# Performance work log

Measured on AMD Instinct MI355X. Metric: run time of the kernel, lower is better.

Reference implementation:

```python
import jax, jax.numpy as jnp
import numpy as np

B, L, S, D = 64, 1024, 8, 128  # batch, seq len, num_snapshots, feat dim


def setup_inputs() -> dict:
    key = jax.random.key(0)
    ks = jax.random.split(key, 12)
    src_ids = jax.random.randint(ks[0], (B, L), 0, 2000, dtype=jnp.int32)
    dst_ids = jax.random.randint(ks[1], (B, L), 0, 2000, dtype=jnp.int32)
    # snapshot ids are 1..S in the original code (indexing uses snaps - 1)
    src_snaps = jax.random.randint(ks[2], (B, L), 1, S + 1, dtype=jnp.int32)
    dst_snaps = jax.random.randint(ks[3], (B, L), 1, S + 1, dtype=jnp.int32)
    def lin(k, fan_in, shape):
        return jax.random.uniform(k, shape, jnp.float32, -1.0, 1.0) / np.sqrt(fan_in)
    params = {
        # AggregateSnapshots MLP: Linear(S, D) -> ReLU -> Linear(D, 2)
        'agg_w1': lin(ks[4], S, (S, D)), 'agg_b1': lin(ks[5], S, (D,)),
        'agg_w2': lin(ks[6], D, (D, 2)), 'agg_b2': lin(ks[7], D, (2,)),
        # neighbor_intersect_encode_layer: Linear(1, D) -> ReLU -> Linear(D, D)
        'enc_w1': lin(ks[8], 1, (1, D)), 'enc_b1': lin(ks[9], 1, (D,)),
        'enc_w2': lin(ks[10], D, (D, D)), 'enc_b2': lin(ks[11], D, (D,)),
    }
    return dict(src_padded_nodes_neighbor_ids=src_ids,
                dst_padded_nodes_neighbor_ids=dst_ids,
                src_padded_nodes_snapshots=src_snaps,
                dst_padded_nodes_snapshots=dst_snaps,
                num_snapshots=S, **params)


def _match_counts(ids_a, sn_a, ids_b, sn_b):
    # counts[i, j] = #{k : ids_b[i,k] == ids_a[i,j] and sn_b[i,k] == sn_a[i,j]}
    eq = (ids_a[:, :, None] == ids_b[:, None, :]) & (sn_a[:, :, None] == sn_b[:, None, :])
    return eq.sum(axis=-1).astype(jnp.float32)  # [B, L]


def _intersects(ids, sn, other_ids, other_sn, num_snapshots):
    self_cnt = _match_counts(ids, sn, ids, sn)            # [B, L]
    cross_cnt = _match_counts(ids, sn, other_ids, other_sn)
    valid = (ids != 0).astype(jnp.float32)                # padding rows stay zero
    oh = jax.nn.one_hot(sn - 1, num_snapshots, dtype=jnp.float32)  # [B, L, S]
    cnts = jnp.stack([self_cnt, cross_cnt], axis=2)       # [B, L, 2]
    return (cnts * valid[:, :, None])[..., None] * oh[:, :, None, :]  # [B, L, 2, S]


def _agg_mlp(x, w1, b1, w2, b2):
    # x: [B, L, 2, S] -> Linear(S,D) -> ReLU -> Linear(D,2) -> reshape(B,L,2,2) -> mean over dim 2
    h = jax.nn.relu(jnp.einsum('blcs,sd->blcd', x, w1) + b1)
    y = jnp.einsum('blcd,de->blce', h, w2) + b2           # [B, L, 2, 2]
    return y.mean(axis=2)                                 # [B, L, 2]


def _encode(y, w1, b1, w2, b2):
    # y: [B, L, 2] -> unsqueeze(-1) -> Linear(1,D) -> ReLU -> Linear(D,D) -> sum over dim 2
    h = jax.nn.relu(y[..., None] * w1[0] + b1)            # [B, L, 2, D]
    z = jnp.einsum('blcd,de->blce', h, w2) + b2
    return z.sum(axis=2)                                  # [B, L, D]


def reference(src_padded_nodes_neighbor_ids, dst_padded_nodes_neighbor_ids,
              src_padded_nodes_snapshots, dst_padded_nodes_snapshots, num_snapshots,
              agg_w1, agg_b1, agg_w2, agg_b2, enc_w1, enc_b1, enc_w2, enc_b2):
    src_int = _intersects(src_padded_nodes_neighbor_ids, src_padded_nodes_snapshots,
                          dst_padded_nodes_neighbor_ids, dst_padded_nodes_snapshots, num_snapshots)
    dst_self_cross = _intersects(dst_padded_nodes_neighbor_ids, dst_padded_nodes_snapshots,
                                 src_padded_nodes_neighbor_ids, src_padded_nodes_snapshots, num_snapshots)
    # dst layout: channel 0 = counts from src list, channel 1 = self counts
    dst_int = dst_self_cross[:, :, ::-1, :]
    src_snap_feat = _agg_mlp(src_int, agg_w1, agg_b1, agg_w2, agg_b2)
    dst_snap_feat = _agg_mlp(dst_int, agg_w1, agg_b1, agg_w2, agg_b2)
    src_feat = _encode(src_snap_feat, enc_w1, enc_b1, enc_w2, enc_b2)
    dst_feat = _encode(dst_snap_feat, enc_w1, enc_b1, enc_w2, enc_b2)
    return (src_feat, dst_feat)
```

## Files before the change

kernel.cpp:

```cpp
#include <hip/hip_runtime.h>


#define LSEQ 1024
#define NBATCH 64
#define DDIM 128
#define NKEYS 16384
#define CMAX 16

__global__ __launch_bounds__(1024) void count_kernel(
    const int* __restrict__ src_ids, const int* __restrict__ dst_ids,
    const int* __restrict__ src_sn,  const int* __restrict__ dst_sn,
    unsigned int* __restrict__ cnt_src, unsigned int* __restrict__ cnt_dst)
{
    __shared__ unsigned int hist[NKEYS];
    const int b = blockIdx.x;
    const int t = threadIdx.x;

    for (int i = t; i < NKEYS; i += 1024) hist[i] = 0u;
    __syncthreads();

    const int base = b * LSEQ;
    const int sid = src_ids[base + t];
    const int ssn = src_sn[base + t];
    const int did = dst_ids[base + t];
    const int dsn = dst_sn[base + t];

    unsigned int skey = (unsigned int)(sid * 8 + ((ssn - 1) & 7));
    unsigned int dkey = (unsigned int)(did * 8 + ((dsn - 1) & 7));
    if (skey >= NKEYS) skey = NKEYS - 1;
    if (dkey >= NKEYS) dkey = NKEYS - 1;

    atomicAdd(&hist[skey], 1u);
    atomicAdd(&hist[dkey], 65536u);
    __syncthreads();

    const unsigned int hs = hist[skey];
    const unsigned int hd = hist[dkey];
    const unsigned int s_self  = hs & 0xffffu, s_cross = hs >> 16;
    const unsigned int d_self  = hd >> 16,     d_cross = hd & 0xffffu;
    const unsigned int sv = (sid != 0) ? 1u : 0u;
    const unsigned int dv = (did != 0) ? 1u : 0u;

    cnt_src[base + t] = (s_self * sv) | ((s_cross * sv) << 11)
                        | ((unsigned int)((ssn - 1) & 7) << 22);
    cnt_dst[base + t] = (d_self * dv) | ((d_cross * dv) << 11)
                        | ((unsigned int)((dsn - 1) & 7) << 22);
}

__global__ __launch_bounds__(128) void table_kernel(
    const float* __restrict__ agg_w1, const float* __restrict__ agg_b1,
    const float* __restrict__ agg_w2, const float* __restrict__ agg_b2,
    const float* __restrict__ enc_w1, const float* __restrict__ enc_b1,
    const float* __restrict__ enc_w2, const float* __restrict__ enc_b2,
    float* __restrict__ table)
{
    const int bx = blockIdx.x;
    const int sn = bx >> 8;
    const int c0 = (bx >> 4) & 15;
    const int c1 = bx & 15;
    const int d  = threadIdx.x;

    __shared__ float red0[DDIM], red1[DDIM], g[DDIM];

    const float w1d = agg_w1[sn * DDIM + d];
    const float b1d = agg_b1[d];
    const float h = fmaxf((float)c0 * w1d + b1d, 0.0f)
                  + fmaxf((float)c1 * w1d + b1d, 0.0f);
    red0[d] = h * agg_w2[d * 2 + 0];
    red1[d] = h * agg_w2[d * 2 + 1];
    __syncthreads();
    for (int s = 64; s > 0; s >>= 1) {
        if (d < s) { red0[d] += red0[d + s]; red1[d] += red1[d + s]; }
        __syncthreads();
    }
    const float y0 = agg_b2[0] + 0.5f * red0[0];
    const float y1 = agg_b2[1] + 0.5f * red1[0];
    __syncthreads();

    const float w1e = enc_w1[d], b1e = enc_b1[d];
    g[d] = fmaxf(y0 * w1e + b1e, 0.0f) + fmaxf(y1 * w1e + b1e, 0.0f);
    __syncthreads();

    float acc = 2.0f * enc_b2[d];
    #pragma unroll 8
    for (int k = 0; k < DDIM; ++k)
        acc += g[k] * enc_w2[k * DDIM + d];
    table[bx * DDIM + d] = acc;
}

__global__ __launch_bounds__(256) void gather_kernel(
    const unsigned int* __restrict__ cnt_src,
    const unsigned int* __restrict__ cnt_dst,
    const float* __restrict__ table,
    const float* __restrict__ agg_w1, const float* __restrict__ agg_b1,
    const float* __restrict__ agg_w2, const float* __restrict__ agg_b2,
    const float* __restrict__ enc_w1, const float* __restrict__ enc_b1,
    const float* __restrict__ enc_w2, const float* __restrict__ enc_b2,
    float* __restrict__ out)
{
    const int gt   = blockIdx.x * 256 + threadIdx.x;
    const int unit = gt >> 5;
    const int q    = gt & 31;
    const int side = unit >> 16;
    const int idx  = unit & 65535;

    const unsigned int packed = side ? cnt_dst[idx] : cnt_src[idx];
    const unsigned int c0 = packed & 0x7FFu;
    const unsigned int c1 = (packed >> 11) & 0x7FFu;
    const unsigned int sn = (packed >> 22) & 7u;

    float4 v;
    if (c0 < CMAX && c1 < CMAX) {
        const float4* src = (const float4*)(table
            + ((sn * 256u + c0 * 16u + c1) * DDIM));
        v = src[q];
    } else {
        float s0 = 0.0f, s1 = 0.0f;
        for (int dd = 0; dd < DDIM; ++dd) {
            const float w1d = agg_w1[sn * DDIM + dd];
            const float b1d = agg_b1[dd];
            const float h = fmaxf((float)c0 * w1d + b1d, 0.0f)
                          + fmaxf((float)c1 * w1d + b1d, 0.0f);
            s0 += h * agg_w2[dd * 2 + 0];
            s1 += h * agg_w2[dd * 2 + 1];
        }
        const float y0 = agg_b2[0] + 0.5f * s0;
        const float y1 = agg_b2[1] + 0.5f * s1;
        float o0 = 2.0f * enc_b2[q * 4 + 0];
        float o1 = 2.0f * enc_b2[q * 4 + 1];
        float o2 = 2.0f * enc_b2[q * 4 + 2];
        float o3 = 2.0f * enc_b2[q * 4 + 3];
        for (int k = 0; k < DDIM; ++k) {
            const float w1e = enc_w1[k], b1e = enc_b1[k];
            const float gk = fmaxf(y0 * w1e + b1e, 0.0f)
                           + fmaxf(y1 * w1e + b1e, 0.0f);
            o0 += gk * enc_w2[k * DDIM + q * 4 + 0];
            o1 += gk * enc_w2[k * DDIM + q * 4 + 1];
            o2 += gk * enc_w2[k * DDIM + q * 4 + 2];
            o3 += gk * enc_w2[k * DDIM + q * 4 + 3];
        }
        v = make_float4(o0, o1, o2, o3);
    }
    ((float4*)out)[gt] = v;
}

extern "C" void kernel_launch(void* const* d_in, const int* in_sizes, int n_in,
                              void* d_out, int out_size, void* d_ws, size_t ws_size,
                              hipStream_t stream)
{
    const int* src_ids = (const int*)d_in[0];
    const int* dst_ids = (const int*)d_in[1];
    const int* src_sn  = (const int*)d_in[2];
    const int* dst_sn  = (const int*)d_in[3];
    const float* agg_w1 = (const float*)d_in[5];
    const float* agg_b1 = (const float*)d_in[6];
    const float* agg_w2 = (const float*)d_in[7];
    const float* agg_b2 = (const float*)d_in[8];
    const float* enc_w1 = (const float*)d_in[9];
    const float* enc_b1 = (const float*)d_in[10];
    const float* enc_w2 = (const float*)d_in[11];
    const float* enc_b2 = (const float*)d_in[12];
    float* out = (float*)d_out;

    unsigned int* cnt_src = (unsigned int*)d_ws;
    unsigned int* cnt_dst = cnt_src + NBATCH * LSEQ;
    float* table = (float*)(cnt_dst + NBATCH * LSEQ);

    count_kernel<<<NBATCH, 1024, 0, stream>>>(src_ids, dst_ids, src_sn, dst_sn,
                                              cnt_src, cnt_dst);
    table_kernel<<<8 * CMAX * CMAX, 128, 0, stream>>>(
        agg_w1, agg_b1, agg_w2, agg_b2, enc_w1, enc_b1, enc_w2, enc_b2, table);
    gather_kernel<<<(2 * NBATCH * LSEQ * 32) / 256, 256, 0, stream>>>(
        cnt_src, cnt_dst, table,
        agg_w1, agg_b1, agg_w2, agg_b2, enc_w1, enc_b1, enc_w2, enc_b2, out);
}
```

Baseline: 111.1 us.

## Fuse count, table and gather into one cooperative persistent kernel

Replaces the three launches with one cooperative kernel that runs three phases separated by grid syncs. The phases are: zero a global per-batch histogram and build the lookup table with one wave per entry, fill the histogram with global atomics, then gather. Counts are no longer packed into a staging buffer; the gather recomputes keys from the ids and reads the histogram directly. The goal is to remove launch overhead and serialization between kernels. In exchange it adds a 4 MB global histogram to zero, global-memory atomics in place of LDS atomics, and the cost of grid-wide barriers.

```diff
diff --git a/kernel.cpp b/kernel.cpp
--- a/kernel.cpp
+++ b/kernel.cpp
@@ -1,147 +1,219 @@
 #include <hip/hip_runtime.h>
-
-
-#define LSEQ 1024
-#define NBATCH 64
-#define DDIM 128
-#define NKEYS 16384
-#define CMAX 16
-
-__global__ __launch_bounds__(1024) void count_kernel(
-    const int* __restrict__ src_ids, const int* __restrict__ dst_ids,
-    const int* __restrict__ src_sn,  const int* __restrict__ dst_sn,
-    unsigned int* __restrict__ cnt_src, unsigned int* __restrict__ cnt_dst)
-{
-    __shared__ unsigned int hist[NKEYS];
-    const int b = blockIdx.x;
-    const int t = threadIdx.x;
-
-    for (int i = t; i < NKEYS; i += 1024) hist[i] = 0u;
-    __syncthreads();
-
-    const int base = b * LSEQ;
-    const int sid = src_ids[base + t];
-    const int ssn = src_sn[base + t];
-    const int did = dst_ids[base + t];
-    const int dsn = dst_sn[base + t];
-
-    unsigned int skey = (unsigned int)(sid * 8 + ((ssn - 1) & 7));
-    unsigned int dkey = (unsigned int)(did * 8 + ((dsn - 1) & 7));
-    if (skey >= NKEYS) skey = NKEYS - 1;
-    if (dkey >= NKEYS) dkey = NKEYS - 1;
-
-    atomicAdd(&hist[skey], 1u);
-    atomicAdd(&hist[dkey], 65536u);
-    __syncthreads();
-
-    const unsigned int hs = hist[skey];
-    const unsigned int hd = hist[dkey];
-    const unsigned int s_self  = hs & 0xffffu, s_cross = hs >> 16;
-    const unsigned int d_self  = hd >> 16,     d_cross = hd & 0xffffu;
-    const unsigned int sv = (sid != 0) ? 1u : 0u;
-    const unsigned int dv = (did != 0) ? 1u : 0u;
-
-    cnt_src[base + t] = (s_self * sv) | ((s_cross * sv) << 11)
-                        | ((unsigned int)((ssn - 1) & 7) << 22);
-    cnt_dst[base + t] = (d_self * dv) | ((d_cross * dv) << 11)
-                        | ((unsigned int)((dsn - 1) & 7) << 22);
-}
-
-__global__ __launch_bounds__(128) void table_kernel(
-    const float* __restrict__ agg_w1, const float* __restrict__ agg_b1,
-    const float* __restrict__ agg_w2, const float* __restrict__ agg_b2,
-    const float* __restrict__ enc_w1, const float* __restrict__ enc_b1,
-    const float* __restrict__ enc_w2, const float* __restrict__ enc_b2,
-    float* __restrict__ table)
-{
-    const int bx = blockIdx.x;
-    const int sn = bx >> 8;
-    const int c0 = (bx >> 4) & 15;
-    const int c1 = bx & 15;
-    const int d  = threadIdx.x;
-
-    __shared__ float red0[DDIM], red1[DDIM], g[DDIM];
-
-    const float w1d = agg_w1[sn * DDIM + d];
-    const float b1d = agg_b1[d];
-    const float h = fmaxf((float)c0 * w1d + b1d, 0.0f)
-                  + fmaxf((float)c1 * w1d + b1d, 0.0f);
-    red0[d] = h * agg_w2[d * 2 + 0];
-    red1[d] = h * agg_w2[d * 2 + 1];
-    __syncthreads();
-    for (int s = 64; s > 0; s >>= 1) {
-        if (d < s) { red0[d] += red0[d + s]; red1[d] += red1[d + s]; }
-        __syncthreads();
-    }
-    const float y0 = agg_b2[0] + 0.5f * red0[0];
-    const float y1 = agg_b2[1] + 0.5f * red1[0];
-    __syncthreads();
-
-    const float w1e = enc_w1[d], b1e = enc_b1[d];
-    g[d] = fmaxf(y0 * w1e + b1e, 0.0f) + fmaxf(y1 * w1e + b1e, 0.0f);
-    __syncthreads();
-
-    float acc = 2.0f * enc_b2[d];
-    #pragma unroll 8
-    for (int k = 0; k < DDIM; ++k)
-        acc += g[k] * enc_w2[k * DDIM + d];
-    table[bx * DDIM + d] = acc;
-}
-
-__global__ __launch_bounds__(256) void gather_kernel(
-    const unsigned int* __restrict__ cnt_src,
-    const unsigned int* __restrict__ cnt_dst,
-    const float* __restrict__ table,
-    const float* __restrict__ agg_w1, const float* __restrict__ agg_b1,
-    const float* __restrict__ agg_w2, const float* __restrict__ agg_b2,
-    const float* __restrict__ enc_w1, const float* __restrict__ enc_b1,
-    const float* __restrict__ enc_w2, const float* __restrict__ enc_b2,
-    float* __restrict__ out)
-{
-    const int gt   = blockIdx.x * 256 + threadIdx.x;
-    const int unit = gt >> 5;
-    const int q    = gt & 31;
-    const int side = unit >> 16;
-    const int idx  = unit & 65535;
-
-    const unsigned int packed = side ? cnt_dst[idx] : cnt_src[idx];
-    const unsigned int c0 = packed & 0x7FFu;
-    const unsigned int c1 = (packed >> 11) & 0x7FFu;
-    const unsigned int sn = (packed >> 22) & 7u;
-
-    float4 v;
-    if (c0 < CMAX && c1 < CMAX) {
-        const float4* src = (const float4*)(table
-            + ((sn * 256u + c0 * 16u + c1) * DDIM));
-        v = src[q];
-    } else {
-        float s0 = 0.0f, s1 = 0.0f;
-        for (int dd = 0; dd < DDIM; ++dd) {
-            const float w1d = agg_w1[sn * DDIM + dd];
-            const float b1d = agg_b1[dd];
+#include <hip/hip_cooperative_groups.h>
+
+namespace cg = cooperative_groups;
+
+
+#define LSEQ    1024
+#define NBATCH  64
+#define DDIM    128
+#define NKEYS   16384
+#define CMAX    16
+#define NTHREADS 256
+#define MAXBLOCKS 1024
+#define NUNITS  (2 * NBATCH * LSEQ)
+#define NQUADS  (NUNITS * (DDIM / 4))
+
+__device__ __forceinline__ void slow_path(
+    unsigned int c0, unsigned int c1, unsigned int snz, int q,
+    const float* __restrict__ agg_w1, const float* __restrict__ agg_b1,
+    const float* __restrict__ agg_w2, const float* __restrict__ agg_b2,
+    const float* __restrict__ enc_w1, const float* __restrict__ enc_b1,
+    const float* __restrict__ enc_w2, const float* __restrict__ enc_b2,
+    float4* v)
+{
+    float s0 = 0.0f, s1 = 0.0f;
+    for (int dd = 0; dd < DDIM; ++dd) {
+        const float w1d = agg_w1[snz * DDIM + dd];
+        const float b1d = agg_b1[dd];
+        const float h = fmaxf((float)c0 * w1d + b1d, 0.0f)
+                      + fmaxf((float)c1 * w1d + b1d, 0.0f);
+        s0 += h * agg_w2[dd * 2 + 0];
+        s1 += h * agg_w2[dd * 2 + 1];
+    }
+    const float y0 = agg_b2[0] + 0.5f * s0;
+    const float y1 = agg_b2[1] + 0.5f * s1;
+    float o0 = 2.0f * enc_b2[q * 4 + 0];
+    float o1 = 2.0f * enc_b2[q * 4 + 1];
+    float o2 = 2.0f * enc_b2[q * 4 + 2];
+    float o3 = 2.0f * enc_b2[q * 4 + 3];
+    for (int k = 0; k < DDIM; ++k) {
+        const float w1e = enc_w1[k], b1e = enc_b1[k];
+        const float gk = fmaxf(y0 * w1e + b1e, 0.0f)
+                       + fmaxf(y1 * w1e + b1e, 0.0f);
+        o0 += gk * enc_w2[k * DDIM + q * 4 + 0];
+        o1 += gk * enc_w2[k * DDIM + q * 4 + 1];
+        o2 += gk * enc_w2[k * DDIM + q * 4 + 2];
+        o3 += gk * enc_w2[k * DDIM + q * 4 + 3];
+    }
+    *v = make_float4(o0, o1, o2, o3);
+}
+
+__device__ __forceinline__ void phase_zero_table(
+    int tid, int stride,
+    const float* __restrict__ agg_w1, const float* __restrict__ agg_b1,
+    const float* __restrict__ agg_w2, const float* __restrict__ agg_b2,
+    const float* __restrict__ enc_w1, const float* __restrict__ enc_b1,
+    const float* __restrict__ enc_w2, const float* __restrict__ enc_b2,
+    unsigned int* __restrict__ hist, float* __restrict__ table)
+{
+    uint4* h4 = (uint4*)hist;
+    const uint4 z = make_uint4(0u, 0u, 0u, 0u);
+    for (int i = tid; i < (NBATCH * NKEYS) / 4; i += stride) h4[i] = z;
+
+    const int lane = threadIdx.x & 63;
+    const int nwaves = stride >> 6;
+    for (int r = tid >> 6; r < 8 * CMAX * CMAX; r += nwaves) {
+        const int sn = r >> 8;
+        const int c0 = (r >> 4) & 15;
+        const int c1 = r & 15;
+        float p0 = 0.0f, p1 = 0.0f;
+        #pragma unroll
+        for (int half = 0; half < 2; ++half) {
+            const int d = lane + half * 64;
+            const float w1d = agg_w1[sn * DDIM + d];
+            const float b1d = agg_b1[d];
             const float h = fmaxf((float)c0 * w1d + b1d, 0.0f)
                           + fmaxf((float)c1 * w1d + b1d, 0.0f);
-            s0 += h * agg_w2[dd * 2 + 0];
-            s1 += h * agg_w2[dd * 2 + 1];
-        }
-        const float y0 = agg_b2[0] + 0.5f * s0;
-        const float y1 = agg_b2[1] + 0.5f * s1;
-        float o0 = 2.0f * enc_b2[q * 4 + 0];
-        float o1 = 2.0f * enc_b2[q * 4 + 1];
-        float o2 = 2.0f * enc_b2[q * 4 + 2];
-        float o3 = 2.0f * enc_b2[q * 4 + 3];
+            p0 += h * agg_w2[d * 2 + 0];
+            p1 += h * agg_w2[d * 2 + 1];
+        }
+        #pragma unroll
+        for (int m = 32; m; m >>= 1) {
+            p0 += __shfl_xor(p0, m, 64);
+            p1 += __shfl_xor(p1, m, 64);
+        }
+        const float y0 = agg_b2[0] + 0.5f * p0;
+        const float y1 = agg_b2[1] + 0.5f * p1;
+        float a0 = 2.0f * enc_b2[lane];
+        float a1 = 2.0f * enc_b2[lane + 64];
+        #pragma unroll 4
         for (int k = 0; k < DDIM; ++k) {
             const float w1e = enc_w1[k], b1e = enc_b1[k];
             const float gk = fmaxf(y0 * w1e + b1e, 0.0f)
                            + fmaxf(y1 * w1e + b1e, 0.0f);
-            o0 += gk * enc_w2[k * DDIM + q * 4 + 0];
-            o1 += gk * enc_w2[k * DDIM + q * 4 + 1];
-            o2 += gk * enc_w2[k * DDIM + q * 4 + 2];
-            o3 += gk * enc_w2[k * DDIM + q * 4 + 3];
-        }
-        v = make_float4(o0, o1, o2, o3);
-    }
-    ((float4*)out)[gt] = v;
+            a0 += gk * enc_w2[k * DDIM + lane];
+            a1 += gk * enc_w2[k * DDIM + lane + 64];
+        }
+        table[r * DDIM + lane]      = a0;
+        table[r * DDIM + lane + 64] = a1;
+    }
+}
+
+__device__ __forceinline__ void phase_hist(
+    int tid, int stride,
+    const int* __restrict__ src_ids, const int* __restrict__ dst_ids,
+    const int* __restrict__ src_sn,  const int* __restrict__ dst_sn,
+    unsigned int* __restrict__ hist)
+{
+    for (int i = tid; i < NUNITS; i += stride) {
+        const int side = i >> 16;
+        const int idx  = i & 65535;
+        const int id = side ? dst_ids[idx] : src_ids[idx];
+        const int sn = side ? dst_sn[idx]  : src_sn[idx];
+        unsigned int key = (unsigned int)(id * 8 + ((sn - 1) & 7));
+        if (key >= NKEYS) key = NKEYS - 1;
+        atomicAdd(&hist[(idx >> 10) * NKEYS + key], side ? 65536u : 1u);
+    }
+}
+
+__device__ __forceinline__ void phase_gather(
+    int tid, int stride,
+    const int* __restrict__ src_ids, const int* __restrict__ dst_ids,
+    const int* __restrict__ src_sn,  const int* __restrict__ dst_sn,
+    const unsigned int* __restrict__ hist, const float* __restrict__ table,
+    const float* __restrict__ agg_w1, const float* __restrict__ agg_b1,
+    const float* __restrict__ agg_w2, const float* __restrict__ agg_b2,
+    const float* __restrict__ enc_w1, const float* __restrict__ enc_b1,
+    const float* __restrict__ enc_w2, const float* __restrict__ enc_b2,
+    float* __restrict__ out)
+{
+    float4* out4 = (float4*)out;
+    #pragma unroll 2
+    for (int gt = tid; gt < NQUADS; gt += stride) {
+        const int unit = gt >> 5;
+        const int q    = gt & 31;
+        const int side = unit >> 16;
+        const int idx  = unit & 65535;
+        const int id = side ? dst_ids[idx] : src_ids[idx];
+        const int sn = side ? dst_sn[idx]  : src_sn[idx];
+        const unsigned int snz = (unsigned int)((sn - 1) & 7);
+        unsigned int key = (unsigned int)(id * 8 + snz);
+        if (key >= NKEYS) key = NKEYS - 1;
+        const unsigned int h = hist[(idx >> 10) * NKEYS + key];
+        const unsigned int lo = h & 0xffffu, hi = h >> 16;
+        const unsigned int valid = (id != 0) ? 1u : 0u;
+        const unsigned int c0 = (side ? hi : lo) * valid;
+        const unsigned int c1 = (side ? lo : hi) * valid;
+
+        float4 v;
+        if (c0 < CMAX && c1 < CMAX) {
+            v = ((const float4*)(table
+                + ((snz * 16u + c0) * 16u + c1) * DDIM))[q];
+        } else {
+            slow_path(c0, c1, snz, q, agg_w1, agg_b1, agg_w2, agg_b2,
+                      enc_w1, enc_b1, enc_w2, enc_b2, &v);
+        }
+        out4[gt] = v;
+    }
+}
+
+__global__ __launch_bounds__(NTHREADS, 4) void fused_kernel(
+    const int* __restrict__ src_ids, const int* __restrict__ dst_ids,
+    const int* __restrict__ src_sn,  const int* __restrict__ dst_sn,
+    const float* __restrict__ agg_w1, const float* __restrict__ agg_b1,
+    const float* __restrict__ agg_w2, const float* __restrict__ agg_b2,
+    const float* __restrict__ enc_w1, const float* __restrict__ enc_b1,
+    const float* __restrict__ enc_w2, const float* __restrict__ enc_b2,
+    unsigned int* __restrict__ hist, float* __restrict__ table,
+    float* __restrict__ out)
+{
+    const int tid    = blockIdx.x * NTHREADS + threadIdx.x;
+    const int stride = gridDim.x * NTHREADS;
+
+    phase_zero_table(tid, stride, agg_w1, agg_b1, agg_w2, agg_b2,
+                     enc_w1, enc_b1, enc_w2, enc_b2, hist, table);
+    cg::this_grid().sync();
+    phase_hist(tid, stride, src_ids, dst_ids, src_sn, dst_sn, hist);
+    cg::this_grid().sync();
+    phase_gather(tid, stride, src_ids, dst_ids, src_sn, dst_sn, hist, table,
+                 agg_w1, agg_b1, agg_w2, agg_b2,
+                 enc_w1, enc_b1, enc_w2, enc_b2, out);
+}
+
+__global__ __launch_bounds__(NTHREADS, 4) void k_zero_table(
+    const float* __restrict__ agg_w1, const float* __restrict__ agg_b1,
+    const float* __restrict__ agg_w2, const float* __restrict__ agg_b2,
+    const float* __restrict__ enc_w1, const float* __restrict__ enc_b1,
+    const float* __restrict__ enc_w2, const float* __restrict__ enc_b2,
+    unsigned int* __restrict__ hist, float* __restrict__ table)
+{
+    phase_zero_table(blockIdx.x * NTHREADS + threadIdx.x, gridDim.x * NTHREADS,
+                     agg_w1, agg_b1, agg_w2, agg_b2,
+                     enc_w1, enc_b1, enc_w2, enc_b2, hist, table);
+}
+__global__ __launch_bounds__(NTHREADS, 4) void k_hist(
+    const int* __restrict__ src_ids, const int* __restrict__ dst_ids,
+    const int* __restrict__ src_sn,  const int* __restrict__ dst_sn,
+    unsigned int* __restrict__ hist)
+{
+    phase_hist(blockIdx.x * NTHREADS + threadIdx.x, gridDim.x * NTHREADS,
+               src_ids, dst_ids, src_sn, dst_sn, hist);
+}
+__global__ __launch_bounds__(NTHREADS, 4) void k_gather(
+    const int* __restrict__ src_ids, const int* __restrict__ dst_ids,
+    const int* __restrict__ src_sn,  const int* __restrict__ dst_sn,
+    const unsigned int* __restrict__ hist, const float* __restrict__ table,
+    const float* __restrict__ agg_w1, const float* __restrict__ agg_b1,
+    const float* __restrict__ agg_w2, const float* __restrict__ agg_b2,
+    const float* __restrict__ enc_w1, const float* __restrict__ enc_b1,
+    const float* __restrict__ enc_w2, const float* __restrict__ enc_b2,
+    float* __restrict__ out)
+{
+    phase_gather(blockIdx.x * NTHREADS + threadIdx.x, gridDim.x * NTHREADS,
+                 src_ids, dst_ids, src_sn, dst_sn, hist, table,
+                 agg_w1, agg_b1, agg_w2, agg_b2,
+                 enc_w1, enc_b1, enc_w2, enc_b2, out);
 }
 
 extern "C" void kernel_launch(void* const* d_in, const int* in_sizes, int n_in,
@@ -162,15 +234,39 @@
     const float* enc_b2 = (const float*)d_in[12];
     float* out = (float*)d_out;
 
-    unsigned int* cnt_src = (unsigned int*)d_ws;
-    unsigned int* cnt_dst = cnt_src + NBATCH * LSEQ;
-    float* table = (float*)(cnt_dst + NBATCH * LSEQ);
-
-    count_kernel<<<NBATCH, 1024, 0, stream>>>(src_ids, dst_ids, src_sn, dst_sn,
-                                              cnt_src, cnt_dst);
-    table_kernel<<<8 * CMAX * CMAX, 128, 0, stream>>>(
-        agg_w1, agg_b1, agg_w2, agg_b2, enc_w1, enc_b1, enc_w2, enc_b2, table);
-    gather_kernel<<<(2 * NBATCH * LSEQ * 32) / 256, 256, 0, stream>>>(
-        cnt_src, cnt_dst, table,
-        agg_w1, agg_b1, agg_w2, agg_b2, enc_w1, enc_b1, enc_w2, enc_b2, out);
-}
+    unsigned int* hist = (unsigned int*)d_ws;
+    float* table = (float*)(hist + NBATCH * NKEYS);
+
+    int maxb = 0;
+    hipError_t qerr = hipOccupancyMaxActiveBlocksPerMultiprocessor(
+        &maxb, fused_kernel, NTHREADS, 0);
+    int grid = MAXBLOCKS;
+    if (qerr == hipSuccess && maxb > 0) {
+        const int cap = maxb * 256;
+        if (cap < grid) grid = cap;
+    } else {
+        grid = 512;
+    }
+
+    void* kargs[] = {
+        (void*)&src_ids, (void*)&dst_ids, (void*)&src_sn, (void*)&dst_sn,
+        (void*)&agg_w1, (void*)&agg_b1, (void*)&agg_w2, (void*)&agg_b2,
+        (void*)&enc_w1, (void*)&enc_b1, (void*)&enc_w2, (void*)&enc_b2,
+        (void*)&hist, (void*)&table, (void*)&out
+    };
+    hipError_t lerr = hipLaunchCooperativeKernel(
+        (void*)fused_kernel, dim3(grid), dim3(NTHREADS), kargs, 0, stream);
+
+    if (lerr != hipSuccess) {
+        (void)hipGetLastError();
+        k_zero_table<<<MAXBLOCKS, NTHREADS, 0, stream>>>(
+            agg_w1, agg_b1, agg_w2, agg_b2,
+            enc_w1, enc_b1, enc_w2, enc_b2, hist, table);
+        k_hist<<<256, NTHREADS, 0, stream>>>(
+            src_ids, dst_ids, src_sn, dst_sn, hist);
+        k_gather<<<MAXBLOCKS * 4, NTHREADS, 0, stream>>>(
+            src_ids, dst_ids, src_sn, dst_sn, hist, table,
+            agg_w1, agg_b1, agg_w2, agg_b2,
+            enc_w1, enc_b1, enc_w2, enc_b2, out);
+    }
+}
```

Measured after the change: 321.8 us. +189.5%, slower.

## Merge count and table kernels into one launch; precompute table row index

Applied to the files above, without the earlier changes.

Merges the histogram-count kernel and the lookup-table kernel into a single launch: some blocks count, the rest build the table with one wave per row and shuffle reductions in place of shared-memory tree reductions. The count stage now emits a precomputed table row index, with a flag bit for out-of-range counts, so the gather does one shift-and-add lookup. The gather processes four quads per thread, moves the rare fallback into a noinline function to reduce register pressure, and uses nontemporal stores for the output. This removes one launch and some address arithmetic. The trade-off is that the combined prep kernel declares the 64KB shared histogram in every block, including the table blocks that never use it, which may limit how many of them run at once.

```diff
diff --git a/kernel.cpp b/kernel.cpp
--- a/kernel.cpp
+++ b/kernel.cpp
@@ -1,96 +1,155 @@
 #include <hip/hip_runtime.h>
 
 
-#define LSEQ 1024
-#define NBATCH 64
-#define DDIM 128
-#define NKEYS 16384
-#define CMAX 16
-
-__global__ __launch_bounds__(1024) void count_kernel(
+#define LSEQ    1024
+#define NBATCH  64
+#define DDIM    128
+#define NKEYS   16384
+#define CMAX    16
+#define NUNITS  (2 * NBATCH * LSEQ)
+#define NQUADS  (NUNITS * (DDIM / 4))
+
+__global__ __launch_bounds__(1024) void prep_kernel(
     const int* __restrict__ src_ids, const int* __restrict__ dst_ids,
     const int* __restrict__ src_sn,  const int* __restrict__ dst_sn,
-    unsigned int* __restrict__ cnt_src, unsigned int* __restrict__ cnt_dst)
-{
-    __shared__ unsigned int hist[NKEYS];
-    const int b = blockIdx.x;
-    const int t = threadIdx.x;
-
-    for (int i = t; i < NKEYS; i += 1024) hist[i] = 0u;
-    __syncthreads();
-
-    const int base = b * LSEQ;
-    const int sid = src_ids[base + t];
-    const int ssn = src_sn[base + t];
-    const int did = dst_ids[base + t];
-    const int dsn = dst_sn[base + t];
-
-    unsigned int skey = (unsigned int)(sid * 8 + ((ssn - 1) & 7));
-    unsigned int dkey = (unsigned int)(did * 8 + ((dsn - 1) & 7));
-    if (skey >= NKEYS) skey = NKEYS - 1;
-    if (dkey >= NKEYS) dkey = NKEYS - 1;
-
-    atomicAdd(&hist[skey], 1u);
-    atomicAdd(&hist[dkey], 65536u);
-    __syncthreads();
-
-    const unsigned int hs = hist[skey];
-    const unsigned int hd = hist[dkey];
-    const unsigned int s_self  = hs & 0xffffu, s_cross = hs >> 16;
-    const unsigned int d_self  = hd >> 16,     d_cross = hd & 0xffffu;
-    const unsigned int sv = (sid != 0) ? 1u : 0u;
-    const unsigned int dv = (did != 0) ? 1u : 0u;
-
-    cnt_src[base + t] = (s_self * sv) | ((s_cross * sv) << 11)
-                        | ((unsigned int)((ssn - 1) & 7) << 22);
-    cnt_dst[base + t] = (d_self * dv) | ((d_cross * dv) << 11)
-                        | ((unsigned int)((dsn - 1) & 7) << 22);
-}
-
-__global__ __launch_bounds__(128) void table_kernel(
     const float* __restrict__ agg_w1, const float* __restrict__ agg_b1,
     const float* __restrict__ agg_w2, const float* __restrict__ agg_b2,
     const float* __restrict__ enc_w1, const float* __restrict__ enc_b1,
     const float* __restrict__ enc_w2, const float* __restrict__ enc_b2,
-    float* __restrict__ table)
-{
-    const int bx = blockIdx.x;
-    const int sn = bx >> 8;
-    const int c0 = (bx >> 4) & 15;
-    const int c1 = bx & 15;
-    const int d  = threadIdx.x;
-
-    __shared__ float red0[DDIM], red1[DDIM], g[DDIM];
-
-    const float w1d = agg_w1[sn * DDIM + d];
-    const float b1d = agg_b1[d];
-    const float h = fmaxf((float)c0 * w1d + b1d, 0.0f)
-                  + fmaxf((float)c1 * w1d + b1d, 0.0f);
-    red0[d] = h * agg_w2[d * 2 + 0];
-    red1[d] = h * agg_w2[d * 2 + 1];
-    __syncthreads();
-    for (int s = 64; s > 0; s >>= 1) {
-        if (d < s) { red0[d] += red0[d + s]; red1[d] += red1[d + s]; }
+    unsigned int* __restrict__ rowinfo, float* __restrict__ table)
+{
+    __shared__ unsigned int hist[NKEYS];
+
+    if (blockIdx.x < NBATCH) {
+        const int b = blockIdx.x;
+        const int t = threadIdx.x;
+
+        uint4* h4 = (uint4*)hist;
+        const uint4 z = make_uint4(0u, 0u, 0u, 0u);
+        #pragma unroll
+        for (int i = 0; i < NKEYS / 4 / 1024; ++i) h4[t + i * 1024] = z;
         __syncthreads();
-    }
-    const float y0 = agg_b2[0] + 0.5f * red0[0];
-    const float y1 = agg_b2[1] + 0.5f * red1[0];
-    __syncthreads();
-
-    const float w1e = enc_w1[d], b1e = enc_b1[d];
-    g[d] = fmaxf(y0 * w1e + b1e, 0.0f) + fmaxf(y1 * w1e + b1e, 0.0f);
-    __syncthreads();
-
-    float acc = 2.0f * enc_b2[d];
-    #pragma unroll 8
-    for (int k = 0; k < DDIM; ++k)
-        acc += g[k] * enc_w2[k * DDIM + d];
-    table[bx * DDIM + d] = acc;
+
+        const int base = b * LSEQ;
+        const int sid = src_ids[base + t];
+        const int ssn = src_sn[base + t];
+        const int did = dst_ids[base + t];
+        const int dsn = dst_sn[base + t];
+
+        const unsigned int ssnz = (unsigned int)((ssn - 1) & 7);
+        const unsigned int dsnz = (unsigned int)((dsn - 1) & 7);
+        unsigned int skey = (unsigned int)(sid * 8) + ssnz;
+        unsigned int dkey = (unsigned int)(did * 8) + dsnz;
+        if (skey >= NKEYS) skey = NKEYS - 1;
+        if (dkey >= NKEYS) dkey = NKEYS - 1;
+
+        atomicAdd(&hist[skey], 1u);
+        atomicAdd(&hist[dkey], 65536u);
+        __syncthreads();
+
+        const unsigned int hs = hist[skey];
+        const unsigned int hd = hist[dkey];
+        const unsigned int sv = (sid != 0) ? 1u : 0u;
+        const unsigned int dv = (did != 0) ? 1u : 0u;
+        const unsigned int sc0 = (hs & 0xffffu) * sv;
+        const unsigned int sc1 = (hs >> 16) * sv;
+        const unsigned int dc0 = (hd >> 16) * dv;
+        const unsigned int dc1 = (hd & 0xffffu) * dv;
+
+        unsigned int si, di;
+        if (sc0 < CMAX && sc1 < CMAX)
+            si = (ssnz << 8) | (sc0 << 4) | sc1;
+        else
+            si = 0x80000000u | sc0 | (sc1 << 11) | (ssnz << 22);
+        if (dc0 < CMAX && dc1 < CMAX)
+            di = (dsnz << 8) | (dc0 << 4) | dc1;
+        else
+            di = 0x80000000u | dc0 | (dc1 << 11) | (dsnz << 22);
+
+        rowinfo[base + t]                   = si;
+        rowinfo[NBATCH * LSEQ + base + t]   = di;
+    } else {
+        const int wave = threadIdx.x >> 6;
+        const int lane = threadIdx.x & 63;
+        const int r = (blockIdx.x - NBATCH) * 16 + wave;
+        const int sn = r >> 8;
+        const int c0 = (r >> 4) & 15;
+        const int c1 = r & 15;
+
+        float p0 = 0.0f, p1 = 0.0f;
+        #pragma unroll
+        for (int half = 0; half < 2; ++half) {
+            const int d = lane + half * 64;
+            const float w1d = agg_w1[sn * DDIM + d];
+            const float b1d = agg_b1[d];
+            const float h = fmaxf((float)c0 * w1d + b1d, 0.0f)
+                          + fmaxf((float)c1 * w1d + b1d, 0.0f);
+            p0 += h * agg_w2[d * 2 + 0];
+            p1 += h * agg_w2[d * 2 + 1];
+        }
+        #pragma unroll
+        for (int m = 32; m; m >>= 1) {
+            p0 += __shfl_xor(p0, m, 64);
+            p1 += __shfl_xor(p1, m, 64);
+        }
+        const float y0 = agg_b2[0] + 0.5f * p0;
+        const float y1 = agg_b2[1] + 0.5f * p1;
+
+        float a0 = 2.0f * enc_b2[lane];
+        float a1 = 2.0f * enc_b2[lane + 64];
+        #pragma unroll 4
+        for (int k = 0; k < DDIM; ++k) {
+            const float w1e = enc_w1[k], b1e = enc_b1[k];
+            const float gk = fmaxf(y0 * w1e + b1e, 0.0f)
+                           + fmaxf(y1 * w1e + b1e, 0.0f);
+            a0 += gk * enc_w2[k * DDIM + lane];
+            a1 += gk * enc_w2[k * DDIM + lane + 64];
+        }
+        table[r * DDIM + lane]      = a0;
+        table[r * DDIM + lane + 64] = a1;
+    }
+}
+
+__device__ __noinline__ void slow_path(
+    unsigned int info, int q,
+    const float* __restrict__ agg_w1, const float* __restrict__ agg_b1,
+    const float* __restrict__ agg_w2, const float* __restrict__ agg_b2,
+    const float* __restrict__ enc_w1, const float* __restrict__ enc_b1,
+    const float* __restrict__ enc_w2, const float* __restrict__ enc_b2,
+    float4* v)
+{
+    const unsigned int c0  = info & 0x7FFu;
+    const unsigned int c1  = (info >> 11) & 0x7FFu;
+    const unsigned int snz = (info >> 22) & 7u;
+    float s0 = 0.0f, s1 = 0.0f;
+    for (int dd = 0; dd < DDIM; ++dd) {
+        const float w1d = agg_w1[snz * DDIM + dd];
+        const float b1d = agg_b1[dd];
+        const float h = fmaxf((float)c0 * w1d + b1d, 0.0f)
+                      + fmaxf((float)c1 * w1d + b1d, 0.0f);
+        s0 += h * agg_w2[dd * 2 + 0];
+        s1 += h * agg_w2[dd * 2 + 1];
+    }
+    const float y0 = agg_b2[0] + 0.5f * s0;
+    const float y1 = agg_b2[1] + 0.5f * s1;
+    float o0 = 2.0f * enc_b2[q * 4 + 0];
+    float o1 = 2.0f * enc_b2[q * 4 + 1];
+    float o2 = 2.0f * enc_b2[q * 4 + 2];
+    float o3 = 2.0f * enc_b2[q * 4 + 3];
+    for (int k = 0; k < DDIM; ++k) {
+        const float w1e = enc_w1[k], b1e = enc_b1[k];
+        const float gk = fmaxf(y0 * w1e + b1e, 0.0f)
+                       + fmaxf(y1 * w1e + b1e, 0.0f);
+        o0 += gk * enc_w2[k * DDIM + q * 4 + 0];
+        o1 += gk * enc_w2[k * DDIM + q * 4 + 1];
+        o2 += gk * enc_w2[k * DDIM + q * 4 + 2];
+        o3 += gk * enc_w2[k * DDIM + q * 4 + 3];
+    }
+    *v = make_float4(o0, o1, o2, o3);
 }
 
 __global__ __launch_bounds__(256) void gather_kernel(
-    const unsigned int* __restrict__ cnt_src,
-    const unsigned int* __restrict__ cnt_dst,
+    const unsigned int* __restrict__ rowinfo,
     const float* __restrict__ table,
     const float* __restrict__ agg_w1, const float* __restrict__ agg_b1,
     const float* __restrict__ agg_w2, const float* __restrict__ agg_b2,
@@ -98,50 +157,28 @@
     const float* __restrict__ enc_w2, const float* __restrict__ enc_b2,
     float* __restrict__ out)
 {
-    const int gt   = blockIdx.x * 256 + threadIdx.x;
-    const int unit = gt >> 5;
-    const int q    = gt & 31;
-    const int side = unit >> 16;
-    const int idx  = unit & 65535;
-
-    const unsigned int packed = side ? cnt_dst[idx] : cnt_src[idx];
-    const unsigned int c0 = packed & 0x7FFu;
-    const unsigned int c1 = (packed >> 11) & 0x7FFu;
-    const unsigned int sn = (packed >> 22) & 7u;
-
-    float4 v;
-    if (c0 < CMAX && c1 < CMAX) {
-        const float4* src = (const float4*)(table
-            + ((sn * 256u + c0 * 16u + c1) * DDIM));
-        v = src[q];
-    } else {
-        float s0 = 0.0f, s1 = 0.0f;
-        for (int dd = 0; dd < DDIM; ++dd) {
-            const float w1d = agg_w1[sn * DDIM + dd];
-            const float b1d = agg_b1[dd];
-            const float h = fmaxf((float)c0 * w1d + b1d, 0.0f)
-                          + fmaxf((float)c1 * w1d + b1d, 0.0f);
-            s0 += h * agg_w2[dd * 2 + 0];
-            s1 += h * agg_w2[dd * 2 + 1];
-        }
-        const float y0 = agg_b2[0] + 0.5f * s0;
-        const float y1 = agg_b2[1] + 0.5f * s1;
-        float o0 = 2.0f * enc_b2[q * 4 + 0];
-        float o1 = 2.0f * enc_b2[q * 4 + 1];
-        float o2 = 2.0f * enc_b2[q * 4 + 2];
-        float o3 = 2.0f * enc_b2[q * 4 + 3];
-        for (int k = 0; k < DDIM; ++k) {
-            const float w1e = enc_w1[k], b1e = enc_b1[k];
-            const float gk = fmaxf(y0 * w1e + b1e, 0.0f)
-                           + fmaxf(y1 * w1e + b1e, 0.0f);
-            o0 += gk * enc_w2[k * DDIM + q * 4 + 0];
-            o1 += gk * enc_w2[k * DDIM + q * 4 + 1];
-            o2 += gk * enc_w2[k * DDIM + q * 4 + 2];
-            o3 += gk * enc_w2[k * DDIM + q * 4 + 3];
-        }
-        v = make_float4(o0, o1, o2, o3);
-    }
-    ((float4*)out)[gt] = v;
+    const float4* table4 = (const float4*)table;
+    float4* out4 = (float4*)out;
+    const int base = blockIdx.x * 1024 + threadIdx.x;
+
+    #pragma unroll
+    for (int k = 0; k < 4; ++k) {
+        const int gt   = base + k * 256;
+        const int unit = gt >> 5;
+        const int q    = gt & 31;
+        const unsigned int info = rowinfo[unit];
+        float4 v;
+        if (!(info & 0x80000000u)) {
+            v = table4[(info << 5) + q];
+        } else {
+            slow_path(info, q, agg_w1, agg_b1, agg_w2, agg_b2,
+                      enc_w1, enc_b1, enc_w2, enc_b2, &v);
+        }
+        __builtin_nontemporal_store(v.x, &out4[gt].x);
+        __builtin_nontemporal_store(v.y, &out4[gt].y);
+        __builtin_nontemporal_store(v.z, &out4[gt].z);
+        __builtin_nontemporal_store(v.w, &out4[gt].w);
+    }
 }
 
 extern "C" void kernel_launch(void* const* d_in, const int* in_sizes, int n_in,
@@ -162,15 +199,17 @@
     const float* enc_b2 = (const float*)d_in[12];
     float* out = (float*)d_out;
 
-    unsigned int* cnt_src = (unsigned int*)d_ws;
-    unsigned int* cnt_dst = cnt_src + NBATCH * LSEQ;
-    float* table = (float*)(cnt_dst + NBATCH * LSEQ);
-
-    count_kernel<<<NBATCH, 1024, 0, stream>>>(src_ids, dst_ids, src_sn, dst_sn,
-                                              cnt_src, cnt_dst);
-    table_kernel<<<8 * CMAX * CMAX, 128, 0, stream>>>(
-        agg_w1, agg_b1, agg_w2, agg_b2, enc_w1, enc_b1, enc_w2, enc_b2, table);
-    gather_kernel<<<(2 * NBATCH * LSEQ * 32) / 256, 256, 0, stream>>>(
-        cnt_src, cnt_dst, table,
-        agg_w1, agg_b1, agg_w2, agg_b2, enc_w1, enc_b1, enc_w2, enc_b2, out);
-}
+    unsigned int* rowinfo = (unsigned int*)d_ws;
+    float* table = (float*)(rowinfo + NUNITS);
+
+    prep_kernel<<<NBATCH + 128, 1024, 0, stream>>>(
+        src_ids, dst_ids, src_sn, dst_sn,
+        agg_w1, agg_b1, agg_w2, agg_b2,
+        enc_w1, enc_b1, enc_w2, enc_b2,
+        rowinfo, table);
+
+    gather_kernel<<<NQUADS / 1024, 256, 0, stream>>>(
+        rowinfo, table,
+        agg_w1, agg_b1, agg_w2, agg_b2,
+        enc_w1, enc_b1, enc_w2, enc_b2, out);
+}
```

Result: slower. 126.5 us (+13.9%).
